# Kernel tuning notes

Hardware: AMD Instinct MI355X
Metric: run time of the kernel (lower is better)

The kernel has to match this reference:

```python
import jax, jax.numpy as jnp
import numpy as np

T, B, I, H, P = 256, 128, 1024, 1024, 512  # seq, batch, input, hidden, proj


def setup_inputs() -> dict:
    key = jax.random.key(0)
    ks = jax.random.split(key, 6)
    s = 1.0 / np.sqrt(H)  # torch LSTM init bound: uniform(-1/sqrt(H), 1/sqrt(H))
    x = jax.random.normal(ks[0], (T, B, I), dtype=jnp.float32)
    h = jax.random.normal(ks[1], (1, B, P), dtype=jnp.float32) * 0.1
    c = jax.random.normal(ks[2], (1, B, H), dtype=jnp.float32) * 0.1
    W_ih = jax.random.uniform(ks[3], (4 * H, I), minval=-s, maxval=s, dtype=jnp.float32)
    W_hh = jax.random.uniform(ks[4], (4 * H, P), minval=-s, maxval=s, dtype=jnp.float32)
    W_hr = jax.random.uniform(ks[5], (P, H), minval=-s, maxval=s, dtype=jnp.float32)
    return {"x": x, "h": h, "c": c, "W_ih": W_ih, "W_hh": W_hh, "W_hr": W_hr}


def _lstm_proj(x, h0, c0, W_ih, W_hh, W_hr):
    # Precompute input contribution to gates for all timesteps: [T,B,4H]
    xg = jnp.einsum('tbi,gi->tbg', x, W_ih)

    def step(carry, xg_t):
        h_t, c_t = carry  # h_t:[B,P], c_t:[B,H]
        gates = xg_t + h_t @ W_hh.T  # [B,4H]
        i, f, g, o = jnp.split(gates, 4, axis=-1)  # torch gate order: i,f,g,o
        i = jax.nn.sigmoid(i)
        f = jax.nn.sigmoid(f)
        g = jnp.tanh(g)
        o = jax.nn.sigmoid(o)
        c_new = f * c_t + i * g
        h_full = o * jnp.tanh(c_new)        # [B,H]
        h_new = h_full @ W_hr.T             # projection -> [B,P]
        return (h_new, c_new), h_new

    (hT, cT), ys = jax.lax.scan(step, (h0[0], c0[0]), xg)
    return ys, hT[None, :, :], cT[None, :, :]


def reference(x, h, c, W_ih, W_hh, W_hr):
    return _lstm_proj(x, h, c, W_ih, W_hh, W_hr)
```

## Files before the change

kernel.cpp:

```cpp
#include <hip/hip_runtime.h>
#include <hip/hip_bf16.h>

#define TS 256
#define BB 128
#define II 1024
#define HH 1024
#define PP 512
#define GG 4096
#define NWG 256
#define WPG 64
#define BT 32
#define HCW 16
#define BSTRIDE 1032
#define RSTRIDE 20
#define SMEM_BYTES (64 * BSTRIDE * 2 + 2 * 64 * RSTRIDE * 4)

typedef __attribute__((ext_vector_type(8))) short bf16x8;
typedef __attribute__((ext_vector_type(4))) float f32x4;

__device__ __forceinline__ short f2bs(float f) {
    __hip_bfloat16 h = __float2bfloat16(f);
    return __builtin_bit_cast(short, h);
}
__device__ __forceinline__ float bs2f(short s) {
    return __bfloat162float(__builtin_bit_cast(__hip_bfloat16, s));
}

__device__ __forceinline__ bf16x8 ld8(const __hip_bfloat16* p) {
    return *(const bf16x8*)p;
}
__device__ __forceinline__ bf16x8 ld8(const float* p) {
    f32x4 lo = *(const f32x4*)p;
    f32x4 hi = *(const f32x4*)(p + 4);
    bf16x8 r;
#pragma unroll
    for (int i = 0; i < 4; ++i) { r[i] = f2bs(lo[i]); r[4 + i] = f2bs(hi[i]); }
    return r;
}

__device__ __forceinline__ void stv(float* p, long i, float v) { p[i] = v; }
__device__ __forceinline__ void stv(__hip_bfloat16* p, long i, float v) { p[i] = __float2bfloat16(v); }

__device__ __forceinline__ void st_bf16_wt(__hip_bfloat16* p, float v) {
    int si = (int)f2bs(v);
    asm volatile("global_store_short %0, %1, off sc0 sc1" :: "v"(p), "v"(si));
}
__device__ __forceinline__ void vm_drain() {
    asm volatile("s_waitcnt vmcnt(0)" ::: "memory");
}

template <typename AT, typename BT_, typename CT>
__global__ __launch_bounds__(256) void mfma_gemm_bt(const AT* __restrict__ A,
                                                    const BT_* __restrict__ B,
                                                    CT* __restrict__ C,
                                                    int M, int N, int K) {
    __shared__ __align__(16) short As[128][40];
    __shared__ __align__(16) short Bsh[128][40];
    const int tid = threadIdx.x;
    const long bm = (long)blockIdx.y * 128;
    const long bn = (long)blockIdx.x * 128;
    const int lane = tid & 63, wv = tid >> 6;
    const int l15 = lane & 15, quad = lane >> 4;
    const int wm = (wv >> 1) * 64, wn = (wv & 1) * 64;
    f32x4 acc[4][4] = {};
    for (int k0 = 0; k0 < K; k0 += 32) {
#pragma unroll
        for (int i = 0; i < 2; ++i) {
            int ch = tid + 256 * i;
            int row = ch >> 2, koff = (ch & 3) * 8;
            *(bf16x8*)&As[row][koff] = ld8(&A[(bm + row) * (long)K + k0 + koff]);
            *(bf16x8*)&Bsh[row][koff] = ld8(&B[(bn + row) * (long)K + k0 + koff]);
        }
        __syncthreads();
        bf16x8 af[4], bfv[4];
#pragma unroll
        for (int t = 0; t < 4; ++t) {
            af[t] = *(const bf16x8*)&As[wm + t * 16 + l15][quad * 8];
            bfv[t] = *(const bf16x8*)&Bsh[wn + t * 16 + l15][quad * 8];
        }
#pragma unroll
        for (int mt = 0; mt < 4; ++mt)
#pragma unroll
            for (int nt = 0; nt < 4; ++nt)
                acc[mt][nt] = __builtin_amdgcn_mfma_f32_16x16x32_bf16(af[mt], bfv[nt], acc[mt][nt], 0, 0, 0);
        __syncthreads();
    }
#pragma unroll
    for (int mt = 0; mt < 4; ++mt)
#pragma unroll
        for (int nt = 0; nt < 4; ++nt)
#pragma unroll
            for (int r = 0; r < 4; ++r) {
                long row = bm + wm + mt * 16 + quad * 4 + r;
                long col = bn + wn + nt * 16 + l15;
                stv(C, row * N + col, acc[mt][nt][r]);
            }
}

template <int K>
__device__ __forceinline__ void rec_mm(const __hip_bfloat16* __restrict__ Abase,
                                       const short* __restrict__ Bs, f32x4* acc,
                                       int l15, int quad, int mt, int kh) {
    constexpr int KH = K / 2;
    constexpr int NI = KH / 32;
    const __hip_bfloat16* ap = Abase + (long)(mt * 16 + l15) * K + kh * KH + quad * 8;
    const short* bp0 = Bs + l15 * BSTRIDE + kh * KH + quad * 8;
    bf16x8 av[NI];
#pragma unroll
    for (int i = 0; i < NI; ++i) av[i] = *(const bf16x8*)(ap + i * 32);
#pragma unroll
    for (int i = 0; i < NI; ++i) {
        const short* bp = bp0 + i * 32;
        acc[0] = __builtin_amdgcn_mfma_f32_16x16x32_bf16(av[i], *(const bf16x8*)(bp), acc[0], 0, 0, 0);
        acc[1] = __builtin_amdgcn_mfma_f32_16x16x32_bf16(av[i], *(const bf16x8*)(bp + 16 * BSTRIDE), acc[1], 0, 0, 0);
        acc[2] = __builtin_amdgcn_mfma_f32_16x16x32_bf16(av[i], *(const bf16x8*)(bp + 32 * BSTRIDE), acc[2], 0, 0, 0);
        acc[3] = __builtin_amdgcn_mfma_f32_16x16x32_bf16(av[i], *(const bf16x8*)(bp + 48 * BSTRIDE), acc[3], 0, 0, 0);
    }
}

__global__ __launch_bounds__(256) void lstm_rec_k(
    const __hip_bfloat16* __restrict__ h0b,
    const float* __restrict__ c0,
    const float* __restrict__ Whh,
    const __hip_bfloat16* __restrict__ Wcomb,
    const __hip_bfloat16* __restrict__ xg,
    __hip_bfloat16* __restrict__ hfull,
    float* __restrict__ cT,
    unsigned* __restrict__ flags) {
    extern __shared__ char smem[];
    short* Bs = (short*)smem;
    float* red = (float*)(smem + 64 * BSTRIDE * 2);

    const int tid = threadIdx.x;
    const int wg = blockIdx.x;
    const int grp = wg >> 6;
    const int jj = wg & 63;
    const int hc0 = jj * HCW;
    const int bt = grp * BT;
    const int lane = tid & 63, wv = tid >> 6;
    const int l15 = lane & 15, quad = lane >> 4;
    const int mt = wv & 1, kh = wv >> 1;
    unsigned* gflag = flags + grp * WPG;
    const int brow = bt + mt * 16 + quad * 4;

    for (int ch = tid; ch < 64 * 64; ch += 256) {
        int row = ch >> 6, koff = (ch & 63) * 8;
        long wr = (long)(row >> 4) * HH + hc0 + (row & 15);
        *(bf16x8*)&Bs[row * BSTRIDE + koff] = ld8(&Whh[wr * PP + koff]);
    }

    float creg[4];
    if (kh == 0) {
#pragma unroll
        for (int r = 0; r < 4; ++r) creg[r] = c0[(long)(brow + r) * HH + hc0 + l15];
    }

    short xr[16];
    auto ldxg = [&](int t) {
        if (kh == 0) {
            const __hip_bfloat16* xgt = xg + (long)t * BB * GG;
#pragma unroll
            for (int g = 0; g < 4; ++g)
#pragma unroll
                for (int r = 0; r < 4; ++r)
                    xr[g * 4 + r] = *(const short*)(xgt + (long)(brow + r) * GG + g * HH + hc0 + l15);
        }
    };

    auto finish = [&](f32x4* acc, int t) {
        if (kh == 1) {
            float* rp = red + (mt * 64 + lane) * RSTRIDE;
#pragma unroll
            for (int g = 0; g < 4; ++g) *(f32x4*)(rp + g * 4) = acc[g];
        }
        __syncthreads();
        if (kh == 0) {
            const float* rp = red + (mt * 64 + lane) * RSTRIDE;
#pragma unroll
            for (int g = 0; g < 4; ++g) acc[g] += *(const f32x4*)(rp + g * 4);
            __hip_bfloat16* hp = hfull + (long)t * BB * HH;
#pragma unroll
            for (int r = 0; r < 4; ++r) {
                float gi = acc[0][r] + bs2f(xr[r]);
                float gf = acc[1][r] + bs2f(xr[4 + r]);
                float gg = acc[2][r] + bs2f(xr[8 + r]);
                float go = acc[3][r] + bs2f(xr[12 + r]);
                float i_ = 1.f / (1.f + expf(-gi));
                float f_ = 1.f / (1.f + expf(-gf));
                float g_ = tanhf(gg);
                float o_ = 1.f / (1.f + expf(-go));
                float c = f_ * creg[r] + i_ * g_;
                creg[r] = c;
                st_bf16_wt(hp + (long)(brow + r) * HH + hc0 + l15, o_ * tanhf(c));
            }
            vm_drain();
        }
    };

    ldxg(0);
    __syncthreads();
    {
        f32x4 acc[4] = {};
        rec_mm<PP>(h0b + (long)bt * PP, Bs, acc, l15, quad, mt, kh);
        finish(acc, 0);
    }
    __syncthreads();
    if (tid == 0) {
        __hip_atomic_store(&gflag[jj], 1u, __ATOMIC_RELAXED, __HIP_MEMORY_SCOPE_AGENT);
    }
    for (int ch = tid; ch < 64 * 128; ch += 256) {
        int row = ch >> 7, koff = (ch & 127) * 8;
        long wr = (long)(row >> 4) * HH + hc0 + (row & 15);
        *(bf16x8*)&Bs[row * BSTRIDE + koff] = *(const bf16x8*)&Wcomb[wr * HH + koff];
    }
    __syncthreads();

    for (int t = 1; t < TS; ++t) {
        ldxg(t);
        if (tid < WPG) {
            const unsigned want = (unsigned)t;
            while (__hip_atomic_load(&gflag[tid], __ATOMIC_RELAXED, __HIP_MEMORY_SCOPE_AGENT) < want)
                __builtin_amdgcn_s_sleep(1);
        }
        if (tid == 0) __builtin_amdgcn_fence(__ATOMIC_ACQUIRE, "agent");
        __syncthreads();
        f32x4 acc[4] = {};
        rec_mm<HH>(hfull + ((long)(t - 1) * BB + bt) * HH, Bs, acc, l15, quad, mt, kh);
        finish(acc, t);
        __syncthreads();
        if (tid == 0 && t < TS - 1) {
            __hip_atomic_store(&gflag[jj], (unsigned)(t + 1), __ATOMIC_RELAXED, __HIP_MEMORY_SCOPE_AGENT);
        }
    }

    if (kh == 0) {
#pragma unroll
        for (int r = 0; r < 4; ++r) cT[(long)(brow + r) * HH + hc0 + l15] = creg[r];
    }
}

__global__ __launch_bounds__(256) void prep_k(const float* __restrict__ h0,
                                              __hip_bfloat16* __restrict__ h0b,
                                              const float* __restrict__ Whr,
                                              float* __restrict__ WhrT,
                                              unsigned* __restrict__ flags) {
    int i = blockIdx.x * 256 + threadIdx.x;
    if (i < NWG) flags[i] = 0u;
    if (i < BB * PP) h0b[i] = __float2bfloat16(h0[i]);
    if (i < PP * HH) {
        int h = i / PP, p = i % PP;
        WhrT[i] = Whr[(long)p * HH + h];
    }
}

__global__ __launch_bounds__(256) void tail_k(const float* __restrict__ ys_last,
                                              float* __restrict__ hT) {
    int i = blockIdx.x * 256 + threadIdx.x;
    hT[i] = ys_last[i];
}

extern "C" void kernel_launch(void* const* d_in, const int* in_sizes, int n_in,
                              void* d_out, int out_size, void* d_ws, size_t ws_size,
                              hipStream_t stream) {
    const float* x   = (const float*)d_in[0];
    const float* h0  = (const float*)d_in[1];
    const float* c0  = (const float*)d_in[2];
    const float* Wih = (const float*)d_in[3];
    const float* Whh = (const float*)d_in[4];
    const float* Whr = (const float*)d_in[5];

    float* out = (float*)d_out;
    float* ys = out;
    float* hT = out + (long)TS * BB * PP;
    float* cT = hT + (long)BB * PP;

    char* ws = (char*)d_ws;
    size_t off = 0;
    __hip_bfloat16* xg = (__hip_bfloat16*)(ws + off);    off += (size_t)TS * BB * GG * 2;
    __hip_bfloat16* hfull = (__hip_bfloat16*)(ws + off); off += (size_t)TS * BB * HH * 2;
    __hip_bfloat16* Wcomb = (__hip_bfloat16*)(ws + off); off += (size_t)GG * HH * 2;
    float* WhrT = (float*)(ws + off);                    off += (size_t)HH * PP * 4;
    __hip_bfloat16* h0b = (__hip_bfloat16*)(ws + off);   off += (size_t)BB * PP * 2;
    unsigned* flags = (unsigned*)(ws + off);             off += 1024;

    static int smem_inited = 0;
    if (!smem_inited) {
        (void)hipFuncSetAttribute(reinterpret_cast<const void*>(lstm_rec_k),
                                  hipFuncAttributeMaxDynamicSharedMemorySize, SMEM_BYTES);
        smem_inited = 1;
    }

    dim3 blk(256);

    prep_k<<<dim3((PP * HH) / 256), blk, 0, stream>>>(h0, h0b, Whr, WhrT, flags);

    mfma_gemm_bt<float, float, __hip_bfloat16>
        <<<dim3(GG / 128, (TS * BB) / 128), blk, 0, stream>>>(x, Wih, xg, TS * BB, GG, II);

    mfma_gemm_bt<float, float, __hip_bfloat16>
        <<<dim3(HH / 128, GG / 128), blk, 0, stream>>>(Whh, WhrT, Wcomb, GG, HH, PP);

    {
        const __hip_bfloat16* a0 = h0b;
        const float* a1 = c0;
        const float* a2 = Whh;
        const __hip_bfloat16* a3 = Wcomb;
        const __hip_bfloat16* a4 = xg;
        __hip_bfloat16* a5 = hfull;
        float* a6 = cT;
        unsigned* a7 = flags;
        void* args[] = {(void*)&a0, (void*)&a1, (void*)&a2, (void*)&a3,
                        (void*)&a4, (void*)&a5, (void*)&a6, (void*)&a7};
        (void)hipLaunchCooperativeKernel(reinterpret_cast<void*>(lstm_rec_k),
                                         dim3(NWG), blk, args, SMEM_BYTES, stream);
    }

    mfma_gemm_bt<__hip_bfloat16, float, float>
        <<<dim3(PP / 128, (TS * BB) / 128), blk, 0, stream>>>(hfull, Whr, ys, TS * BB, PP, HH);

    tail_k<<<dim3((BB * PP) / 256), blk, 0, stream>>>(ys + (long)(TS - 1) * BB * PP, hT);
}
```

Before: 2.911 ms.

## Signal per-wave readiness flags and load h_full with cache-bypassing loads

The persistent recurrent kernel now publishes one readiness flag per (workgroup, M-half) wave directly after that wave drains its stores, instead of a block-wide barrier followed by a single flag. The acquire fence is dropped, and the A-operand (previous h_full) is loaded with sc0 sc1 global loads so that stale cached data is not read. This shortens the per-timestep critical path by removing one __syncthreads and the fence. The flag array doubles and twice as many threads poll. Correctness now rests on the cache-bypass loads rather than an explicit fence.

```diff
diff --git a/kernel.cpp b/kernel.cpp
--- a/kernel.cpp
+++ b/kernel.cpp
@@ -44,6 +44,11 @@
 __device__ __forceinline__ void st_bf16_wt(__hip_bfloat16* p, float v) {
     int si = (int)f2bs(v);
     asm volatile("global_store_short %0, %1, off sc0 sc1" :: "v"(p), "v"(si));
+}
+__device__ __forceinline__ f32x4 ld16_mall(const void* p) {
+    f32x4 r;
+    asm volatile("global_load_dwordx4 %0, %1, off sc0 sc1" : "=&v"(r) : "v"(p));
+    return r;
 }
 __device__ __forceinline__ void vm_drain() {
     asm volatile("s_waitcnt vmcnt(0)" ::: "memory");
@@ -105,16 +110,19 @@
     constexpr int NI = KH / 32;
     const __hip_bfloat16* ap = Abase + (long)(mt * 16 + l15) * K + kh * KH + quad * 8;
     const short* bp0 = Bs + l15 * BSTRIDE + kh * KH + quad * 8;
-    bf16x8 av[NI];
-#pragma unroll
-    for (int i = 0; i < NI; ++i) av[i] = *(const bf16x8*)(ap + i * 32);
+    f32x4 avr[NI];
+#pragma unroll
+    for (int i = 0; i < NI; ++i) avr[i] = ld16_mall(ap + i * 32);
+    asm volatile("s_waitcnt vmcnt(0)" ::: "memory");
+    __builtin_amdgcn_sched_barrier(0);
 #pragma unroll
     for (int i = 0; i < NI; ++i) {
+        bf16x8 av = __builtin_bit_cast(bf16x8, avr[i]);
         const short* bp = bp0 + i * 32;
-        acc[0] = __builtin_amdgcn_mfma_f32_16x16x32_bf16(av[i], *(const bf16x8*)(bp), acc[0], 0, 0, 0);
-        acc[1] = __builtin_amdgcn_mfma_f32_16x16x32_bf16(av[i], *(const bf16x8*)(bp + 16 * BSTRIDE), acc[1], 0, 0, 0);
-        acc[2] = __builtin_amdgcn_mfma_f32_16x16x32_bf16(av[i], *(const bf16x8*)(bp + 32 * BSTRIDE), acc[2], 0, 0, 0);
-        acc[3] = __builtin_amdgcn_mfma_f32_16x16x32_bf16(av[i], *(const bf16x8*)(bp + 48 * BSTRIDE), acc[3], 0, 0, 0);
+        acc[0] = __builtin_amdgcn_mfma_f32_16x16x32_bf16(av, *(const bf16x8*)(bp), acc[0], 0, 0, 0);
+        acc[1] = __builtin_amdgcn_mfma_f32_16x16x32_bf16(av, *(const bf16x8*)(bp + 16 * BSTRIDE), acc[1], 0, 0, 0);
+        acc[2] = __builtin_amdgcn_mfma_f32_16x16x32_bf16(av, *(const bf16x8*)(bp + 32 * BSTRIDE), acc[2], 0, 0, 0);
+        acc[3] = __builtin_amdgcn_mfma_f32_16x16x32_bf16(av, *(const bf16x8*)(bp + 48 * BSTRIDE), acc[3], 0, 0, 0);
     }
 }
 
@@ -140,7 +148,7 @@
     const int lane = tid & 63, wv = tid >> 6;
     const int l15 = lane & 15, quad = lane >> 4;
     const int mt = wv & 1, kh = wv >> 1;
-    unsigned* gflag = flags + grp * WPG;
+    unsigned* gflag = flags + grp * 2 * WPG;
     const int brow = bt + mt * 16 + quad * 4;
 
     for (int ch = tid; ch < 64 * 64; ch += 256) {
@@ -167,7 +175,7 @@
         }
     };
 
-    auto finish = [&](f32x4* acc, int t) {
+    auto finish = [&](f32x4* acc, int t, bool flag) {
         if (kh == 1) {
             float* rp = red + (mt * 64 + lane) * RSTRIDE;
 #pragma unroll
@@ -194,6 +202,10 @@
                 st_bf16_wt(hp + (long)(brow + r) * HH + hc0 + l15, o_ * tanhf(c));
             }
             vm_drain();
+            if (flag && lane == 0) {
+                __hip_atomic_store(&gflag[jj * 2 + mt], (unsigned)(t + 1),
+                                   __ATOMIC_RELAXED, __HIP_MEMORY_SCOPE_AGENT);
+            }
         }
     };
 
@@ -202,11 +214,7 @@
     {
         f32x4 acc[4] = {};
         rec_mm<PP>(h0b + (long)bt * PP, Bs, acc, l15, quad, mt, kh);
-        finish(acc, 0);
-    }
-    __syncthreads();
-    if (tid == 0) {
-        __hip_atomic_store(&gflag[jj], 1u, __ATOMIC_RELAXED, __HIP_MEMORY_SCOPE_AGENT);
+        finish(acc, 0, true);
     }
     for (int ch = tid; ch < 64 * 128; ch += 256) {
         int row = ch >> 7, koff = (ch & 127) * 8;
@@ -217,20 +225,15 @@
 
     for (int t = 1; t < TS; ++t) {
         ldxg(t);
-        if (tid < WPG) {
+        if (tid < 2 * WPG) {
             const unsigned want = (unsigned)t;
             while (__hip_atomic_load(&gflag[tid], __ATOMIC_RELAXED, __HIP_MEMORY_SCOPE_AGENT) < want)
                 __builtin_amdgcn_s_sleep(1);
         }
-        if (tid == 0) __builtin_amdgcn_fence(__ATOMIC_ACQUIRE, "agent");
         __syncthreads();
         f32x4 acc[4] = {};
         rec_mm<HH>(hfull + ((long)(t - 1) * BB + bt) * HH, Bs, acc, l15, quad, mt, kh);
-        finish(acc, t);
-        __syncthreads();
-        if (tid == 0 && t < TS - 1) {
-            __hip_atomic_store(&gflag[jj], (unsigned)(t + 1), __ATOMIC_RELAXED, __HIP_MEMORY_SCOPE_AGENT);
-        }
+        finish(acc, t, t < TS - 1);
     }
 
     if (kh == 0) {
@@ -245,7 +248,7 @@
                                               float* __restrict__ WhrT,
                                               unsigned* __restrict__ flags) {
     int i = blockIdx.x * 256 + threadIdx.x;
-    if (i < NWG) flags[i] = 0u;
+    if (i < 2 * NWG) flags[i] = 0u;
     if (i < BB * PP) h0b[i] = __float2bfloat16(h0[i]);
     if (i < PP * HH) {
         int h = i / PP, p = i % PP;
@@ -281,7 +284,7 @@
     __hip_bfloat16* Wcomb = (__hip_bfloat16*)(ws + off); off += (size_t)GG * HH * 2;
     float* WhrT = (float*)(ws + off);                    off += (size_t)HH * PP * 4;
     __hip_bfloat16* h0b = (__hip_bfloat16*)(ws + off);   off += (size_t)BB * PP * 2;
-    unsigned* flags = (unsigned*)(ws + off);             off += 1024;
+    unsigned* flags = (unsigned*)(ws + off);             off += 4096;
 
     static int smem_inited = 0;
     if (!smem_inited) {
```

New measurement: 3.034 ms. +4.2%, slower.
